# Kernel optimization log

Measured on AMD Instinct MI355X. Metric: run time of the kernel, lower is better.

Reference implementation:

```python
import jax, jax.numpy as jnp
import numpy as np

TWO_PI = 2.0 * np.pi


def setup_inputs() -> dict:
    key = jax.random.key(0)
    k1, k2 = jax.random.split(key)
    B, S, F, U = 16, 1024, 2048, 2048
    x = jax.random.normal(k1, (B, S, F), dtype=jnp.float32)
    # Dense(quantum_projection): weight [2F, U], bias [U]
    W = jax.random.normal(k2, (2 * F, U), dtype=jnp.float32) * (1.0 / np.sqrt(2 * F))
    b = jnp.zeros((U,), dtype=jnp.float32)
    return {"x": x, "W": W, "b": b}


def reference(x, W, b):
    # x: [B, S, F]
    qp = x * TWO_PI                                   # quantum_params
    quantum_enhanced = jnp.tanh(qp) + 0.1 * (jnp.sin(qp) * jnp.cos(qp * 0.5))
    # diag(outer(v, v)) == v**2 -- skip the O(F^2) matmul
    entanglement = quantum_enhanced * quantum_enhanced
    feats = jnp.concatenate([quantum_enhanced, entanglement], axis=-1)  # [B,S,2F]
    out = jnp.tanh(jnp.einsum('bsf,fu->bsu', feats, W) + b)             # [B,S,U]
    return out
```

## Files before the change

### kernel.cpp

```cpp
#include <hip/hip_runtime.h>
#include <hip/hip_bf16.h>
#include <math.h>


typedef __bf16 b16x8 __attribute__((ext_vector_type(8)));
typedef float f32x4 __attribute__((ext_vector_type(4)));

constexpr int Mdim = 16384;
constexpr int Fdim = 2048;
constexpr int Kdim = 4096;
constexpr int Ndim = 2048;

__device__ __forceinline__ float tanh_2pix(float x) {
  float ax = fabsf(x);
  float e = __expf(-12.566370614359172f * ax);
  float t = (1.0f - e) * __builtin_amdgcn_rcpf(1.0f + e);
  return copysignf(t, x);
}

__device__ __forceinline__ float fast_tanh(float x) {
  float ax = fabsf(x);
  float e = __expf(-2.0f * ax);
  float t = (1.0f - e) * __builtin_amdgcn_rcpf(1.0f + e);
  return copysignf(t, x);
}

struct __align__(16) B8 { __bf16 v[8]; };

__global__ void feats_kernel(const float* __restrict__ x, __bf16* __restrict__ feats) {
  int idx = blockIdx.x * blockDim.x + threadIdx.x;
  long i8 = (long)idx << 3;
  float4 xv0 = reinterpret_cast<const float4*>(x)[idx * 2];
  float4 xv1 = reinterpret_cast<const float4*>(x)[idx * 2 + 1];
  float q[8] = {xv0.x, xv0.y, xv0.z, xv0.w, xv1.x, xv1.y, xv1.z, xv1.w};
  B8 qe, en;
#pragma unroll
  for (int j = 0; j < 8; ++j) {
    float xx = q[j];
    float s = __builtin_amdgcn_sinf(xx);
    float c = __builtin_amdgcn_cosf(0.5f * xx);
    float v = tanh_2pix(xx) + 0.1f * s * c;
    qe.v[j] = (__bf16)v;
    en.v[j] = (__bf16)(v * v);
  }
  int m = (int)(i8 >> 11);
  int f = (int)(i8 & (Fdim - 1));
  size_t base = (size_t)m * Kdim + f;
  *reinterpret_cast<B8*>(feats + base) = qe;
  *reinterpret_cast<B8*>(feats + base + Fdim) = en;
}

__global__ void wtrans_kernel(const float* __restrict__ W, __bf16* __restrict__ Wt) {
  __shared__ float tile[32][33];
  int bn = blockIdx.x;
  int bk = blockIdx.y;
  int tx = threadIdx.x;
  int ty = threadIdx.y;
#pragma unroll
  for (int i = 0; i < 4; ++i) {
    int kk = bk * 32 + ty + i * 8;
    tile[ty + i * 8][tx] = W[(size_t)kk * Ndim + bn * 32 + tx];
  }
  __syncthreads();
#pragma unroll
  for (int i = 0; i < 4; ++i) {
    int nn = bn * 32 + ty + i * 8;
    Wt[(size_t)nn * Kdim + bk * 32 + tx] = (__bf16)tile[tx][ty + i * 8];
  }
}

typedef const __attribute__((address_space(1))) void* gptr1;
typedef __attribute__((address_space(3))) void* lptr3;

__device__ __forceinline__ void gld_lds16(const __bf16* g, __bf16* l) {
  __builtin_amdgcn_global_load_lds((gptr1)g, (lptr3)l, 16, 0, 0);
}

__global__ __launch_bounds__(256, 4) void gemm_tanh_kernel(
    const __bf16* __restrict__ A,
    const __bf16* __restrict__ Bt,
    const float* __restrict__ bias,
    float* __restrict__ out) {
  __shared__ __align__(16) __bf16 smem[4 * 4096];
  __bf16* const sA0 = smem;
  __bf16* const sB0 = smem + 4096;
  __bf16* const sA1 = smem + 8192;
  __bf16* const sB1 = smem + 12288;

  const int tid = threadIdx.x;
  const int wv = tid >> 6;
  const int lane = tid & 63;
  const int m0 = blockIdx.y * 128;
  const int n0 = blockIdx.x * 128;

  const int srow = tid >> 2;
  const int scol = (((tid & 3) ^ ((srow >> 1) & 3))) * 8;
  const __bf16* gA0 = A + (size_t)(m0 + srow) * Kdim + scol;
  const __bf16* gA1 = gA0 + (size_t)64 * Kdim;
  const __bf16* gB0 = Bt + (size_t)(n0 + srow) * Kdim + scol;
  const __bf16* gB1 = gB0 + (size_t)64 * Kdim;
  const int ldsoff = wv * 512;

  const int wm = (wv >> 1) * 64;
  const int wn = (wv & 1) * 64;
  const int lr = lane & 15;
  const int lq = lane >> 4;
  const int swz = (lr >> 1) & 3;
  const int kchunk = (lq ^ swz) * 8;

  int aoff[4], boff[4];
#pragma unroll
  for (int i = 0; i < 4; ++i) {
    aoff[i] = (wm + i * 16 + lr) * 32 + kchunk;
    boff[i] = (wn + i * 16 + lr) * 32 + kchunk;
  }

  f32x4 acc[4][4];
#pragma unroll
  for (int i = 0; i < 4; ++i)
#pragma unroll
    for (int j = 0; j < 4; ++j) acc[i][j] = (f32x4){0.f, 0.f, 0.f, 0.f};

  auto stage = [&](int k0, __bf16* dA, __bf16* dB) {
    gld_lds16(gA0 + k0, dA + ldsoff);
    gld_lds16(gA1 + k0, dA + 2048 + ldsoff);
    gld_lds16(gB0 + k0, dB + ldsoff);
    gld_lds16(gB1 + k0, dB + 2048 + ldsoff);
  };
  auto compute = [&](const __bf16* cA, const __bf16* cB) {
    b16x8 av[4], bv[4];
#pragma unroll
    for (int i = 0; i < 4; ++i) av[i] = *reinterpret_cast<const b16x8*>(cA + aoff[i]);
#pragma unroll
    for (int i = 0; i < 4; ++i) bv[i] = *reinterpret_cast<const b16x8*>(cB + boff[i]);
#pragma unroll
    for (int i = 0; i < 4; ++i)
#pragma unroll
      for (int j = 0; j < 4; ++j)
        acc[i][j] = __builtin_amdgcn_mfma_f32_16x16x32_bf16(av[i], bv[j], acc[i][j], 0, 0, 0);
  };

  stage(0, sA0, sB0);
  for (int k0 = 0; k0 < Kdim; k0 += 64) {
    __syncthreads();
    if (k0 + 32 < Kdim) stage(k0 + 32, sA1, sB1);
    compute(sA0, sB0);
    __syncthreads();
    if (k0 + 64 < Kdim) stage(k0 + 64, sA0, sB0);
    compute(sA1, sB1);
  }

#pragma unroll
  for (int j = 0; j < 4; ++j) {
    int gn = n0 + wn + j * 16 + lr;
    float bval = bias[gn];
#pragma unroll
    for (int i = 0; i < 4; ++i) {
      int gmb = m0 + wm + i * 16 + lq * 4;
#pragma unroll
      for (int r = 0; r < 4; ++r) {
        float v = acc[i][j][r] + bval;
        out[(size_t)(gmb + r) * Ndim + gn] = fast_tanh(v);
      }
    }
  }
}

extern "C" void kernel_launch(void* const* d_in, const int* in_sizes, int n_in,
                              void* d_out, int out_size, void* d_ws, size_t ws_size,
                              hipStream_t stream) {
  const float* x = (const float*)d_in[0];
  const float* W = (const float*)d_in[1];
  const float* b = (const float*)d_in[2];
  float* out = (float*)d_out;

  __bf16* Wt = (__bf16*)d_ws;
  __bf16* feats = Wt + (size_t)Ndim * Kdim;

  hipLaunchKernelGGL(feats_kernel, dim3(Mdim * Fdim / 8 / 256), dim3(256), 0,
                     stream, x, feats);
  hipLaunchKernelGGL(wtrans_kernel, dim3(Ndim / 32, Kdim / 32), dim3(32, 8), 0,
                     stream, W, Wt);
  hipLaunchKernelGGL(gemm_tanh_kernel, dim3(Ndim / 128, Mdim / 128), dim3(256),
                     0, stream, feats, Wt, b, out);
}
```

Before: 566.7 us.

## Rewrite GEMM as 256x256 tile with 4-stage LDS pipeline and manual waitcnts

The GEMM moves from 128x128 tiles with 256 threads and double buffering to 256x256 tiles with 512 threads. A four-slot LDS ring is filled by global_load_lds, with hand-placed s_waitcnt and s_barrier calls, MFMA priority raised via s_setprio, and a remapped block order for better L2 reuse. The aim is to raise arithmetic intensity, hide global-load latency, and cut barrier stalls. In exchange it uses 128KB of LDS, more accumulator registers and a fragile hand-scheduled synchronisation sequence.

```diff
diff --git a/kernel.cpp b/kernel.cpp
--- a/kernel.cpp
+++ b/kernel.cpp
@@ -76,91 +76,143 @@
   __builtin_amdgcn_global_load_lds((gptr1)g, (lptr3)l, 16, 0, 0);
 }
 
-__global__ __launch_bounds__(256, 4) void gemm_tanh_kernel(
+#define BARRIER()    asm volatile("s_barrier" ::: "memory")
+#define WAIT_LGKM0() asm volatile("s_waitcnt lgkmcnt(0)" ::: "memory")
+#define WAIT_VM(n)   asm volatile("s_waitcnt vmcnt(" #n ")" ::: "memory")
+
+#define TILE(h, S1, S2, S3, S4) do {                                        \
+    const int s0_ = (h) & 3, s1_ = ((h) + 1) & 3;                           \
+    rdA(s0_, 0); rdB(s0_);                                                  \
+    if (S1) stageA((h) + 3);                                                \
+    BARRIER(); WAIT_LGKM0();                                                \
+    mfma4(0);                                                               \
+    BARRIER();                                                              \
+    rdA(s0_, 4);                                                            \
+    if (S2) stageB((h) + 4);                                                \
+    BARRIER(); WAIT_LGKM0();                                                \
+    mfma4(4);                                                               \
+    BARRIER();                                                              \
+    rdA(s1_, 0); rdB(s1_);                                                  \
+    if (S3) stageA((h) + 4);                                                \
+    BARRIER(); WAIT_LGKM0();                                                \
+    mfma4(0);                                                               \
+    BARRIER();                                                              \
+    rdA(s1_, 4);                                                            \
+    if (S4) stageB((h) + 5);                                                \
+    BARRIER(); WAIT_LGKM0();                                                \
+    mfma4(4);                                                               \
+  } while (0)
+
+__global__ __launch_bounds__(512, 2) void gemm_tanh_kernel(
     const __bf16* __restrict__ A,
     const __bf16* __restrict__ Bt,
     const float* __restrict__ bias,
     float* __restrict__ out) {
-  __shared__ __align__(16) __bf16 smem[4 * 4096];
-  __bf16* const sA0 = smem;
-  __bf16* const sB0 = smem + 4096;
-  __bf16* const sA1 = smem + 8192;
-  __bf16* const sB1 = smem + 12288;
+  __shared__ __align__(16) __bf16 smem[65536];
+  __bf16* const sA = smem;
+  __bf16* const sB = smem + 32768;
 
   const int tid = threadIdx.x;
   const int wv = tid >> 6;
   const int lane = tid & 63;
-  const int m0 = blockIdx.y * 128;
-  const int n0 = blockIdx.x * 128;
-
-  const int srow = tid >> 2;
-  const int scol = (((tid & 3) ^ ((srow >> 1) & 3))) * 8;
-  const __bf16* gA0 = A + (size_t)(m0 + srow) * Kdim + scol;
-  const __bf16* gA1 = gA0 + (size_t)64 * Kdim;
-  const __bf16* gB0 = Bt + (size_t)(n0 + srow) * Kdim + scol;
-  const __bf16* gB1 = gB0 + (size_t)64 * Kdim;
-  const int ldsoff = wv * 512;
-
-  const int wm = (wv >> 1) * 64;
-  const int wn = (wv & 1) * 64;
+
+  const int orig = blockIdx.y * 8 + blockIdx.x;
+  const int wg = (orig & 7) * 64 + (orig >> 3);
+  const int m0 = (wg >> 3) * 256;
+  const int n0 = (wg & 7) * 256;
+
+  const int wm = (wv >> 2) * 128;
+  const int wn = (wv & 3) * 64;
   const int lr = lane & 15;
   const int lq = lane >> 4;
-  const int swz = (lr >> 1) & 3;
-  const int kchunk = (lq ^ swz) * 8;
-
-  int aoff[4], boff[4];
-#pragma unroll
-  for (int i = 0; i < 4; ++i) {
-    aoff[i] = (wm + i * 16 + lr) * 32 + kchunk;
-    boff[i] = (wn + i * 16 + lr) * 32 + kchunk;
-  }
-
-  f32x4 acc[4][4];
-#pragma unroll
-  for (int i = 0; i < 4; ++i)
+
+  const int L0 = wv * 128 + lane;
+  const int L1 = L0 + 64;
+  const int r0 = L0 >> 2, r1 = L1 >> 2;
+  const int c0 = (L0 & 3) ^ ((r0 >> 1) & 3);
+  const int c1 = (L1 & 3) ^ ((r1 >> 1) & 3);
+  const __bf16* gA0 = A + (size_t)(m0 + r0) * Kdim + c0 * 8;
+  const __bf16* gA1 = A + (size_t)(m0 + r1) * Kdim + c1 * 8;
+  const __bf16* gB0 = Bt + (size_t)(n0 + r0) * Kdim + c0 * 8;
+  const __bf16* gB1 = Bt + (size_t)(n0 + r1) * Kdim + c1 * 8;
+  const int d0 = wv * 1024;
+  const int d1 = d0 + 512;
+
+  auto stageA = [&](int h) {
+    __bf16* s = sA + (h & 3) * 8192;
+    gld_lds16(gA0 + h * 32, s + d0);
+    gld_lds16(gA1 + h * 32, s + d1);
+  };
+  auto stageB = [&](int h) {
+    __bf16* s = sB + (h & 3) * 8192;
+    gld_lds16(gB0 + h * 32, s + d0);
+    gld_lds16(gB1 + h * 32, s + d1);
+  };
+
+  const int chunk = (lq ^ ((lr >> 1) & 3)) * 8;
+  const int ard = (wm + lr) * 32 + chunk;
+  const int brd = (wn + lr) * 32 + chunk;
+
+  f32x4 acc[8][4];
+#pragma unroll
+  for (int i = 0; i < 8; ++i)
 #pragma unroll
     for (int j = 0; j < 4; ++j) acc[i][j] = (f32x4){0.f, 0.f, 0.f, 0.f};
 
-  auto stage = [&](int k0, __bf16* dA, __bf16* dB) {
-    gld_lds16(gA0 + k0, dA + ldsoff);
-    gld_lds16(gA1 + k0, dA + 2048 + ldsoff);
-    gld_lds16(gB0 + k0, dB + ldsoff);
-    gld_lds16(gB1 + k0, dB + 2048 + ldsoff);
-  };
-  auto compute = [&](const __bf16* cA, const __bf16* cB) {
-    b16x8 av[4], bv[4];
-#pragma unroll
-    for (int i = 0; i < 4; ++i) av[i] = *reinterpret_cast<const b16x8*>(cA + aoff[i]);
-#pragma unroll
-    for (int i = 0; i < 4; ++i) bv[i] = *reinterpret_cast<const b16x8*>(cB + boff[i]);
+  b16x8 av[4], bv[4];
+  auto rdA = [&](int s, int fb) {
 #pragma unroll
     for (int i = 0; i < 4; ++i)
+      av[i] = *reinterpret_cast<const b16x8*>(sA + s * 8192 + ard + (fb + i) * 512);
+  };
+  auto rdB = [&](int s) {
+#pragma unroll
+    for (int i = 0; i < 4; ++i)
+      bv[i] = *reinterpret_cast<const b16x8*>(sB + s * 8192 + brd + i * 512);
+  };
+  auto mfma4 = [&](int fb) {
+    __builtin_amdgcn_s_setprio(1);
+#pragma unroll
+    for (int i = 0; i < 4; ++i)
 #pragma unroll
       for (int j = 0; j < 4; ++j)
-        acc[i][j] = __builtin_amdgcn_mfma_f32_16x16x32_bf16(av[i], bv[j], acc[i][j], 0, 0, 0);
-  };
-
-  stage(0, sA0, sB0);
-  for (int k0 = 0; k0 < Kdim; k0 += 64) {
-    __syncthreads();
-    if (k0 + 32 < Kdim) stage(k0 + 32, sA1, sB1);
-    compute(sA0, sB0);
-    __syncthreads();
-    if (k0 + 64 < Kdim) stage(k0 + 64, sA0, sB0);
-    compute(sA1, sB1);
-  }
+        acc[fb + i][j] =
+            __builtin_amdgcn_mfma_f32_16x16x32_bf16(av[i], bv[j], acc[fb + i][j], 0, 0, 0);
+    __builtin_amdgcn_s_setprio(0);
+  };
+
+  float bval[4];
+#pragma unroll
+  for (int j = 0; j < 4; ++j) bval[j] = bias[n0 + wn + j * 16 + lr];
+  WAIT_VM(0);
+
+  stageA(0); stageB(0); stageA(1); stageB(1);
+  WAIT_VM(4);
+  stageA(2); stageB(2); stageB(3);
+  WAIT_VM(6);
+  BARRIER();
+
+  for (int u = 0; u < 31; ++u) {
+    const int h = u * 4;
+    TILE(h, 1, 1, 1, 1);
+    WAIT_VM(6); BARRIER();
+    TILE(h + 2, 1, 1, 1, 1);
+    WAIT_VM(6); BARRIER();
+  }
+  TILE(124, 1, 0, 0, 0);
+  WAIT_VM(0); BARRIER();
+  TILE(126, 0, 0, 0, 0);
 
 #pragma unroll
   for (int j = 0; j < 4; ++j) {
-    int gn = n0 + wn + j * 16 + lr;
-    float bval = bias[gn];
-#pragma unroll
-    for (int i = 0; i < 4; ++i) {
-      int gmb = m0 + wm + i * 16 + lq * 4;
+    const int gn = n0 + wn + j * 16 + lr;
+#pragma unroll
+    for (int i = 0; i < 8; ++i) {
+      const int gm = m0 + wm + i * 16 + lq * 4;
 #pragma unroll
       for (int r = 0; r < 4; ++r) {
-        float v = acc[i][j][r] + bval;
-        out[(size_t)(gmb + r) * Ndim + gn] = fast_tanh(v);
+        float v = acc[i][j][r] + bval[j];
+        out[(size_t)(gm + r) * Ndim + gn] = fast_tanh(v);
       }
     }
   }
@@ -181,6 +233,6 @@
                      stream, x, feats);
   hipLaunchKernelGGL(wtrans_kernel, dim3(Ndim / 32, Kdim / 32), dim3(32, 8), 0,
                      stream, W, Wt);
-  hipLaunchKernelGGL(gemm_tanh_kernel, dim3(Ndim / 128, Mdim / 128), dim3(256),
+  hipLaunchKernelGGL(gemm_tanh_kernel, dim3(Ndim / 256, Mdim / 256), dim3(512),
                      0, stream, feats, Wt, b, out);
 }
```

After: 495.0 us. 1.14x faster.

## Enlarge GEMM tile to 256x256 with 4-stage LDS pipeline and block swizzle

Applied to the files above, without the earlier changes.

The GEMM block tile grows from 128x128 to 256x256, so each wave computes a 128x128 sub-tile with 8x8 MFMA accumulators. This raises arithmetic intensity per LDS and global load. LDS buffering goes from double to a 4-slot ring with three stages in flight, using explicit vmcnt waits and raw s_barrier instead of __syncthreads. It also remaps block indices for L2 locality and raises wave priority around the MFMA burst. In exchange, occupancy drops to one block per CU (launch_bounds 256,1) with heavy register and LDS use (128 KB), so spills or poor latency hiding are a risk.

```diff
diff --git a/kernel.cpp b/kernel.cpp
--- a/kernel.cpp
+++ b/kernel.cpp
@@ -76,91 +76,112 @@
   __builtin_amdgcn_global_load_lds((gptr1)g, (lptr3)l, 16, 0, 0);
 }
 
-__global__ __launch_bounds__(256, 4) void gemm_tanh_kernel(
+#define BARRIER()    asm volatile("s_barrier" ::: "memory")
+#define WAIT_LGKM0() asm volatile("s_waitcnt lgkmcnt(0)" ::: "memory")
+#define WAIT_VM(n)   asm volatile("s_waitcnt vmcnt(" #n ")" ::: "memory")
+
+__global__ __launch_bounds__(256, 1) void gemm_tanh_kernel(
     const __bf16* __restrict__ A,
     const __bf16* __restrict__ Bt,
     const float* __restrict__ bias,
     float* __restrict__ out) {
-  __shared__ __align__(16) __bf16 smem[4 * 4096];
-  __bf16* const sA0 = smem;
-  __bf16* const sB0 = smem + 4096;
-  __bf16* const sA1 = smem + 8192;
-  __bf16* const sB1 = smem + 12288;
+  __shared__ __align__(16) __bf16 smem[65536];
+  __bf16* const sA = smem;
+  __bf16* const sB = smem + 32768;
 
   const int tid = threadIdx.x;
   const int wv = tid >> 6;
   const int lane = tid & 63;
-  const int m0 = blockIdx.y * 128;
-  const int n0 = blockIdx.x * 128;
-
-  const int srow = tid >> 2;
-  const int scol = (((tid & 3) ^ ((srow >> 1) & 3))) * 8;
-  const __bf16* gA0 = A + (size_t)(m0 + srow) * Kdim + scol;
-  const __bf16* gA1 = gA0 + (size_t)64 * Kdim;
-  const __bf16* gB0 = Bt + (size_t)(n0 + srow) * Kdim + scol;
-  const __bf16* gB1 = gB0 + (size_t)64 * Kdim;
-  const int ldsoff = wv * 512;
-
-  const int wm = (wv >> 1) * 64;
-  const int wn = (wv & 1) * 64;
+
+  const int orig = blockIdx.y * 8 + blockIdx.x;
+  const int wg = (orig & 7) * 64 + (orig >> 3);
+  const int m0 = (wg >> 3) * 256;
+  const int n0 = (wg & 7) * 256;
+
+  const int wm = (wv >> 1) * 128;
+  const int wn = (wv & 1) * 128;
   const int lr = lane & 15;
   const int lq = lane >> 4;
-  const int swz = (lr >> 1) & 3;
-  const int kchunk = (lq ^ swz) * 8;
-
-  int aoff[4], boff[4];
-#pragma unroll
-  for (int i = 0; i < 4; ++i) {
-    aoff[i] = (wm + i * 16 + lr) * 32 + kchunk;
-    boff[i] = (wn + i * 16 + lr) * 32 + kchunk;
-  }
-
-  f32x4 acc[4][4];
-#pragma unroll
-  for (int i = 0; i < 4; ++i)
-#pragma unroll
-    for (int j = 0; j < 4; ++j) acc[i][j] = (f32x4){0.f, 0.f, 0.f, 0.f};
-
-  auto stage = [&](int k0, __bf16* dA, __bf16* dB) {
-    gld_lds16(gA0 + k0, dA + ldsoff);
-    gld_lds16(gA1 + k0, dA + 2048 + ldsoff);
-    gld_lds16(gB0 + k0, dB + ldsoff);
-    gld_lds16(gB1 + k0, dB + 2048 + ldsoff);
+
+  const __bf16* gA[4];
+  const __bf16* gB[4];
+  int dstoff[4];
+#pragma unroll
+  for (int q = 0; q < 4; ++q) {
+    int L = wv * 256 + q * 64 + lane;
+    int r = L >> 2;
+    int c = (L & 3) ^ ((r >> 1) & 3);
+    gA[q] = A + (size_t)(m0 + r) * Kdim + c * 8;
+    gB[q] = Bt + (size_t)(n0 + r) * Kdim + c * 8;
+    dstoff[q] = wv * 2048 + q * 512;
+  }
+
+  auto stage = [&](int h) {
+    const int sl = (h & 3) * 8192;
+#pragma unroll
+    for (int q = 0; q < 4; ++q) gld_lds16(gA[q] + h * 32, sA + sl + dstoff[q]);
+#pragma unroll
+    for (int q = 0; q < 4; ++q) gld_lds16(gB[q] + h * 32, sB + sl + dstoff[q]);
   };
-  auto compute = [&](const __bf16* cA, const __bf16* cB) {
-    b16x8 av[4], bv[4];
-#pragma unroll
-    for (int i = 0; i < 4; ++i) av[i] = *reinterpret_cast<const b16x8*>(cA + aoff[i]);
-#pragma unroll
-    for (int i = 0; i < 4; ++i) bv[i] = *reinterpret_cast<const b16x8*>(cB + boff[i]);
-#pragma unroll
-    for (int i = 0; i < 4; ++i)
-#pragma unroll
-      for (int j = 0; j < 4; ++j)
+
+  const int chunk = (lq ^ ((lr >> 1) & 3)) * 8;
+  const int ard = (wm + lr) * 32 + chunk;
+  const int brd = (wn + lr) * 32 + chunk;
+
+  f32x4 acc[8][8];
+#pragma unroll
+  for (int i = 0; i < 8; ++i)
+#pragma unroll
+    for (int j = 0; j < 8; ++j) acc[i][j] = (f32x4){0.f, 0.f, 0.f, 0.f};
+
+  b16x8 av[8], bv[8];
+
+  float bval[8];
+#pragma unroll
+  for (int j = 0; j < 8; ++j) bval[j] = bias[n0 + wn + j * 16 + lr];
+  WAIT_VM(0);
+
+  stage(0); stage(1); stage(2);
+
+  for (int h = 0; h < 128; ++h) {
+    if (h < 126) {
+      WAIT_VM(16);
+    } else if (h == 126) {
+      WAIT_VM(8);
+    } else {
+      WAIT_VM(0);
+    }
+    WAIT_LGKM0();
+    BARRIER();
+    if (h <= 124) stage(h + 3);
+
+    const int sl = (h & 3) * 8192;
+#pragma unroll
+    for (int i = 0; i < 8; ++i)
+      av[i] = *reinterpret_cast<const b16x8*>(sA + sl + ard + i * 512);
+#pragma unroll
+    for (int i = 0; i < 8; ++i)
+      bv[i] = *reinterpret_cast<const b16x8*>(sB + sl + brd + i * 512);
+
+    __builtin_amdgcn_s_setprio(1);
+#pragma unroll
+    for (int j = 0; j < 8; ++j)
+#pragma unroll
+      for (int i = 0; i < 8; ++i)
         acc[i][j] = __builtin_amdgcn_mfma_f32_16x16x32_bf16(av[i], bv[j], acc[i][j], 0, 0, 0);
-  };
-
-  stage(0, sA0, sB0);
-  for (int k0 = 0; k0 < Kdim; k0 += 64) {
-    __syncthreads();
-    if (k0 + 32 < Kdim) stage(k0 + 32, sA1, sB1);
-    compute(sA0, sB0);
-    __syncthreads();
-    if (k0 + 64 < Kdim) stage(k0 + 64, sA0, sB0);
-    compute(sA1, sB1);
-  }
-
-#pragma unroll
-  for (int j = 0; j < 4; ++j) {
-    int gn = n0 + wn + j * 16 + lr;
-    float bval = bias[gn];
-#pragma unroll
-    for (int i = 0; i < 4; ++i) {
-      int gmb = m0 + wm + i * 16 + lq * 4;
+    __builtin_amdgcn_s_setprio(0);
+  }
+
+#pragma unroll
+  for (int j = 0; j < 8; ++j) {
+    const int gn = n0 + wn + j * 16 + lr;
+#pragma unroll
+    for (int i = 0; i < 8; ++i) {
+      const int gm = m0 + wm + i * 16 + lq * 4;
 #pragma unroll
       for (int r = 0; r < 4; ++r) {
-        float v = acc[i][j][r] + bval;
-        out[(size_t)(gmb + r) * Ndim + gn] = fast_tanh(v);
+        float v = acc[i][j][r] + bval[j];
+        out[(size_t)(gm + r) * Ndim + gn] = fast_tanh(v);
       }
     }
   }
@@ -181,6 +202,6 @@
                      stream, x, feats);
   hipLaunchKernelGGL(wtrans_kernel, dim3(Ndim / 32, Kdim / 32), dim3(32, 8), 0,
                      stream, W, Wt);
-  hipLaunchKernelGGL(gemm_tanh_kernel, dim3(Ndim / 128, Mdim / 128), dim3(256),
+  hipLaunchKernelGGL(gemm_tanh_kernel, dim3(Ndim / 256, Mdim / 256), dim3(256),
                      0, stream, feats, Wt, b, out);
 }
```

New measurement: 975.0 us. +72.0%, slower.
